# Performance work log

Measured on AMD Instinct MI355X. Metric: run time of the kernel, lower is better.

Reference implementation:

```python
import jax, jax.numpy as jnp
import numpy as np

N = 1000; K = 500; M = N - K          # codeword / info / parity bits
NUE = 4; NBS = 4                      # tx / rx antennas
BPS = 4; RATE = 0.5; NSYM = N // BPS  # 16-QAM, 250 symbols per codeword
NITER = 5                             # BP iterations

# 16-QAM constellation, Gray-coded per axis (Sionna-style), unit energy
_bits = ((np.arange(16)[:, None] >> np.array([3, 2, 1, 0])) & 1).astype(np.float32)
_re = (1 - 2 * _bits[:, 0]) * (2 - (1 - 2 * _bits[:, 2]))
_im = (1 - 2 * _bits[:, 1]) * (2 - (1 - 2 * _bits[:, 3]))
POINTS = jnp.asarray((_re + 1j * _im) / np.sqrt(10.0), dtype=jnp.complex64)  # [16]
LABELS = jnp.asarray(_bits)  # [16,4] bit labels per point


def setup_inputs() -> dict:
    key = jax.random.key(0)
    ks = jax.random.split(key, 5)
    batch = 1000
    # systematic sparse LDPC-like code: H = [P^T | I_M], info-bit degree 3
    rs = np.random.RandomState(0)
    P = np.zeros((K, M), np.int32)
    for i in range(K):
        P[i, rs.choice(M, 3, replace=False)] = 1
    vi, ci = np.nonzero(P)
    vn = np.concatenate([vi, K + np.arange(M)]).astype(np.int32)  # [2000]
    cn = np.concatenate([ci, np.arange(M)]).astype(np.int32)      # [2000]
    b = jax.random.randint(ks[0], (batch, NUE, K), 0, 2, dtype=jnp.int32)
    h_re = jax.random.normal(ks[1], (batch * NSYM, NBS, NUE), jnp.float32)
    h_im = jax.random.normal(ks[2], (batch * NSYM, NBS, NUE), jnp.float32)
    n_re = jax.random.normal(ks[3], (batch * NSYM, NBS), jnp.float32)
    n_im = jax.random.normal(ks[4], (batch * NSYM, NBS), jnp.float32)
    return {"batch_size": batch, "ebno_db": jnp.full((1,), 5.0, jnp.float32),
            "b": b, "P": jnp.asarray(P), "cn_idx": jnp.asarray(cn),
            "vn_idx": jnp.asarray(vn), "h_re": h_re, "h_im": h_im,
            "noise_re": n_re, "noise_im": n_im}


def _forward(batch_size, ebno_db, b, P, cn_idx, vn_idx, h_re, h_im, noise_re, noise_im):
    no = 1.0 / (10.0 ** (ebno_db[0] / 10.0) * BPS * RATE)  # ebnodb2no
    # --- LDPC encode (systematic): c = [b, b@P mod 2] ---
    bf = b.astype(jnp.float32)
    parity = jnp.mod(jnp.round(bf @ P.astype(jnp.float32)), 2.0)
    c = jnp.concatenate([bf, parity], -1)                    # [B,NUE,N]
    # --- QAM mapper ---
    idx = (c.reshape(batch_size, NUE, NSYM, BPS) @ jnp.array([8., 4., 2., 1.], jnp.float32)).astype(jnp.int32)
    x = POINTS[idx]                                          # [B,NUE,NSYM]
    x_f = jnp.transpose(x, (0, 2, 1)).reshape(-1, NUE)       # [B*NSYM,NUE]
    # --- flat fading channel, h ~ CN(0,1), AWGN ---
    h = ((h_re + 1j * h_im) / np.sqrt(2.0)).astype(jnp.complex64)
    w = ((noise_re + 1j * noise_im) * jnp.sqrt(no / 2.0)).astype(jnp.complex64)
    y = jnp.einsum('bij,bj->bi', h, x_f) + w                 # [B*NSYM,NBS]
    # --- LMMSE equalizer: G = H^H (H H^H + no I)^-1, unbiased scaling ---
    A = jnp.einsum('bik,bjk->bij', h, jnp.conj(h)) \
        + no.astype(jnp.complex64) * jnp.eye(NBS, dtype=jnp.complex64)
    Ainv_y = jnp.linalg.solve(A, y[..., None])[..., 0]
    x_raw = jnp.einsum('bij,bi->bj', jnp.conj(h), Ainv_y)    # G y, [B*NSYM,NUE]
    GH = jnp.einsum('bij,bik->bjk', jnp.conj(h), jnp.linalg.solve(A, h))
    d = jnp.real(jnp.diagonal(GH, axis1=1, axis2=2))         # diag(GH), [B*NSYM,NUE]
    x_hat = x_raw / d.astype(jnp.complex64)
    no_eff = jnp.maximum(1.0 / d - 1.0, 1e-12)
    x_hat = jnp.transpose(x_hat.reshape(batch_size, NSYM, NUE), (0, 2, 1))  # [B,NUE,NSYM]
    nvar = jnp.transpose(no_eff.reshape(batch_size, NSYM, NUE), (0, 2, 1))
    # --- max-log demapper, L = log p(b=0)/p(b=1) ---
    metric = -(jnp.abs(x_hat[..., None] - POINTS) ** 2) / nvar[..., None]   # [B,NUE,NSYM,16]
    NEG = jnp.float32(-1e30)
    m5 = metric[..., None, :]                               # [B,NUE,NSYM,1,16]
    lab = LABELS.T[None, None, None]                        # [1,1,1,4,16]
    m0 = jnp.max(jnp.where(lab == 0, m5, NEG), -1)
    m1 = jnp.max(jnp.where(lab == 1, m5, NEG), -1)
    llr = (m0 - m1).reshape(batch_size, NUE, N)
    # --- LDPC BP decoder (sum-product over fixed sparse Tanner graph) ---
    Lch = llr.reshape(batch_size * NUE, N).T                # [N, Bc]
    c2v = jnp.zeros((cn_idx.shape[0], Lch.shape[1]), jnp.float32)  # [E, Bc]
    for _ in range(NITER):
        vtot = Lch.at[vn_idx].add(c2v)                      # Lch + segment_sum(c2v)
        m_vc = vtot[vn_idx] - c2v                           # extrinsic VN->CN
        t = jnp.tanh(jnp.clip(m_vc * 0.5, -9.9, 9.9))
        t = jnp.where(t >= 0, jnp.maximum(t, 1e-7), jnp.minimum(t, -1e-7))
        prod = jax.ops.segment_prod(t, cn_idx, num_segments=M)
        c2v = 2.0 * jnp.arctanh(jnp.clip(prod[cn_idx] / t, -0.999999, 0.999999))
    vtot = Lch.at[vn_idx].add(c2v)
    b_hat = (vtot[:K].T < 0).astype(jnp.float32).reshape(batch_size, NUE, K)
    return bf, b_hat


def reference(batch_size, ebno_db, b, P, cn_idx, vn_idx, h_re, h_im, noise_re, noise_im):
    return _forward(batch_size, ebno_db, b, P, cn_idx, vn_idx,
                    h_re, h_im, noise_re, noise_im)
```

## Files before the change

kernel.cpp:

```cpp
#include <hip/hip_runtime.h>
#include <math.h>

#define KK     500
#define MM     500
#define NNODES 1000
#define NSYM   250
#define NITERS 5
#define MAXVDEG 4
#define EMAX   2048
#define TB     256

__global__ void __launch_bounds__(512)
k_setup(const int* __restrict__ cn, const int* __restrict__ vn, int E,
        const float* __restrict__ ebno, const int* __restrict__ P,
        const int* __restrict__ b, int ncw,
        int* __restrict__ cinfo, int* __restrict__ vlist, int* __restrict__ coff,
        double* __restrict__ nobuf, unsigned* __restrict__ Ppack,
        unsigned* __restrict__ bpack, float* __restrict__ out, int packBlocks) {
  __shared__ int sdeg[512];
  __shared__ int ssc[512];
  __shared__ int scur[512];
  __shared__ int svc[NNODES];
  int tid = threadIdx.x;
  int bx = blockIdx.x;

  if (bx == 0) {
    sdeg[tid] = 0;
    for (int n = tid; n < NNODES; n += 512) svc[n] = 0;
    __syncthreads();
    for (int e = tid; e < E; e += 512) atomicAdd(&sdeg[cn[e]], 1);
    __syncthreads();
    int v = sdeg[tid];
    ssc[tid] = v;
    __syncthreads();
    for (int o = 1; o < 512; o <<= 1) {
      int x = (tid >= o) ? ssc[tid - o] : 0;
      __syncthreads();
      ssc[tid] += x;
      __syncthreads();
    }
    int excl = ssc[tid] - v;
    scur[tid] = excl;
    if (tid < MM) {
      coff[tid] = excl;
      if (tid == MM - 1) coff[MM] = ssc[tid];
    }
    __syncthreads();
    for (int e = tid; e < E; e += 512) {
      int c = cn[e], n = vn[e];
      int slot = atomicAdd(&scur[c], 1);
      cinfo[slot] = (c << 16) | n;
      int t = atomicAdd(&svc[n], 1);
      if (t < MAXVDEG) vlist[n * MAXVDEG + t] = slot;
    }
    if (tid == 0) {
      double no = 1.0 / (pow(10.0, (double)ebno[0] * 0.1) * 2.0);
      nobuf[0] = no;
      nobuf[1] = sqrt(no * 0.5);
    }
    return;
  }

  if (bx <= packBlocks) {
    int id = (bx - 1) * 512 + tid;
    if (id < MM * 16) {
      int j = id >> 4, w = id & 15;
      unsigned word = 0u;
      int base = w * 32;
      for (int bit = 0; bit < 32; ++bit) {
        int i = base + bit;
        if (i < KK && P[i * MM + j] != 0) word |= (1u << bit);
      }
      Ppack[j * 16 + w] = word;
    } else {
      int id2 = id - MM * 16;
      if (id2 < ncw * 16) {
        int cw = id2 >> 4, w = id2 & 15;
        unsigned word = 0u;
        int base = w * 32;
        for (int bit = 0; bit < 32; ++bit) {
          int i = base + bit;
          if (i < KK && b[cw * KK + i] != 0) word |= (1u << bit);
        }
        bpack[cw * 16 + w] = word;
      }
    }
    return;
  }

  int id = (bx - 1 - packBlocks) * 512 + tid;
  if (id < ncw * KK) out[id] = (float)b[id];
}

__device__ __forceinline__ void qam_point(int p, double& re, double& im) {
  const double s = 0.31622776601683794;
  int b0 = (p >> 3) & 1, b1 = (p >> 2) & 1, b2 = (p >> 1) & 1, b3 = p & 1;
  re = (double)((1 - 2 * b0) * (2 - (1 - 2 * b2))) * s;
  im = (double)((1 - 2 * b1) * (2 - (1 - 2 * b3))) * s;
}

__global__ void __launch_bounds__(256, 1)
k_lmmse(const float* __restrict__ h_re, const float* __restrict__ h_im,
        const float* __restrict__ n_re, const float* __restrict__ n_im,
        const double* __restrict__ nobuf,
        const unsigned* __restrict__ bpack, const unsigned* __restrict__ Ppack,
        float* __restrict__ Lch2, int T, int ncw) {
  int t = blockIdx.x * blockDim.x + threadIdx.x;
  if (t >= T) return;
  int bt = t / NSYM, s = t - bt * NSYM;

  double no = nobuf[0];
  double sq = nobuf[1];
  const double is2 = 0.7071067811865475244;

  double Hr[4][4], Hi[4][4];
  {
    const float4* hr4 = (const float4*)h_re;
    const float4* hi4 = (const float4*)h_im;
    #pragma unroll
    for (int i = 0; i < 4; ++i) {
      float4 a = hr4[t * 4 + i], c = hi4[t * 4 + i];
      Hr[i][0] = (double)a.x * is2; Hr[i][1] = (double)a.y * is2;
      Hr[i][2] = (double)a.z * is2; Hr[i][3] = (double)a.w * is2;
      Hi[i][0] = (double)c.x * is2; Hi[i][1] = (double)c.y * is2;
      Hi[i][2] = (double)c.z * is2; Hi[i][3] = (double)c.w * is2;
    }
  }

  double xr[4], xi[4];
  #pragma unroll
  for (int ue = 0; ue < 4; ++ue) {
    const unsigned* bp = bpack + (bt * 4 + ue) * 16;
    int v = 0;
    #pragma unroll
    for (int k = 0; k < 4; ++k) {
      int n = 4 * s + k;
      int bit;
      if (n < KK) {
        bit = (bp[n >> 5] >> (n & 31)) & 1;
      } else {
        const unsigned* pp = Ppack + (n - KK) * 16;
        int cnt = 0;
        #pragma unroll
        for (int w = 0; w < 16; ++w) cnt += __popc(bp[w] & pp[w]);
        bit = cnt & 1;
      }
      v = (v << 1) | bit;
    }
    qam_point(v, xr[ue], xi[ue]);
  }

  double yr[4], yi[4];
  {
    float4 wr = ((const float4*)n_re)[t];
    float4 wi = ((const float4*)n_im)[t];
    float wrv[4] = {wr.x, wr.y, wr.z, wr.w};
    float wiv[4] = {wi.x, wi.y, wi.z, wi.w};
    #pragma unroll
    for (int i = 0; i < 4; ++i) {
      double ar = (double)wrv[i] * sq;
      double ai = (double)wiv[i] * sq;
      #pragma unroll
      for (int j = 0; j < 4; ++j) {
        ar += Hr[i][j] * xr[j] - Hi[i][j] * xi[j];
        ai += Hr[i][j] * xi[j] + Hi[i][j] * xr[j];
      }
      yr[i] = ar; yi[i] = ai;
    }
  }

  auto dotc = [&](int i, int j, double& ar, double& ai) {
    double r = 0.0, m = 0.0;
    #pragma unroll
    for (int k = 0; k < 4; ++k) {
      r += Hr[i][k] * Hr[j][k] + Hi[i][k] * Hi[j][k];
      m += Hi[i][k] * Hr[j][k] - Hr[i][k] * Hi[j][k];
    }
    ar = r; ai = m;
  };
  double a00, a11, a22, a33, dum;
  double a10r, a10i, a20r, a20i, a21r, a21i, a30r, a30i, a31r, a31i, a32r, a32i;
  dotc(0, 0, a00, dum);  a00 += no;
  dotc(1, 0, a10r, a10i);
  dotc(1, 1, a11, dum);  a11 += no;
  dotc(2, 0, a20r, a20i);
  dotc(2, 1, a21r, a21i);
  dotc(2, 2, a22, dum);  a22 += no;
  dotc(3, 0, a30r, a30i);
  dotc(3, 1, a31r, a31i);
  dotc(3, 2, a32r, a32i);
  dotc(3, 3, a33, dum);  a33 += no;

  double L00 = sqrt(a00);
  double i00 = 1.0 / L00;
  double L10r = a10r * i00, L10i = a10i * i00;
  double L20r = a20r * i00, L20i = a20i * i00;
  double L30r = a30r * i00, L30i = a30i * i00;
  double L11 = sqrt(a11 - (L10r * L10r + L10i * L10i));
  double i11 = 1.0 / L11;
  double L21r = (a21r - (L20r * L10r + L20i * L10i)) * i11;
  double L21i = (a21i - (L20i * L10r - L20r * L10i)) * i11;
  double L31r = (a31r - (L30r * L10r + L30i * L10i)) * i11;
  double L31i = (a31i - (L30i * L10r - L30r * L10i)) * i11;
  double L22 = sqrt(a22 - (L20r * L20r + L20i * L20i) - (L21r * L21r + L21i * L21i));
  double i22 = 1.0 / L22;
  double L32r = (a32r - (L30r * L20r + L30i * L20i) - (L31r * L21r + L31i * L21i)) * i22;
  double L32i = (a32i - (L30i * L20r - L30r * L20i) - (L31i * L21r - L31r * L21i)) * i22;
  double L33 = sqrt(a33 - (L30r * L30r + L30i * L30i) - (L31r * L31r + L31i * L31i)
                        - (L32r * L32r + L32i * L32i));
  double i33 = 1.0 / L33;

  #pragma unroll
  for (int j = 0; j < 4; ++j) {
    double u0r = Hr[0][j] * i00,               u0i = Hi[0][j] * i00;
    double u1r = (Hr[1][j] - (L10r * u0r - L10i * u0i)) * i11;
    double u1i = (Hi[1][j] - (L10r * u0i + L10i * u0r)) * i11;
    double u2r = (Hr[2][j] - (L20r * u0r - L20i * u0i) - (L21r * u1r - L21i * u1i)) * i22;
    double u2i = (Hi[2][j] - (L20r * u0i + L20i * u0r) - (L21r * u1i + L21i * u1r)) * i22;
    double u3r = (Hr[3][j] - (L30r * u0r - L30i * u0i) - (L31r * u1r - L31i * u1i)
                           - (L32r * u2r - L32i * u2i)) * i33;
    double u3i = (Hi[3][j] - (L30r * u0i + L30i * u0r) - (L31r * u1i + L31i * u1r)
                           - (L32r * u2i + L32i * u2r)) * i33;
    Hr[0][j] = u0r; Hi[0][j] = u0i; Hr[1][j] = u1r; Hi[1][j] = u1i;
    Hr[2][j] = u2r; Hi[2][j] = u2i; Hr[3][j] = u3r; Hi[3][j] = u3i;
  }
  {
    double v0r = yr[0] * i00,               v0i = yi[0] * i00;
    double v1r = (yr[1] - (L10r * v0r - L10i * v0i)) * i11;
    double v1i = (yi[1] - (L10r * v0i + L10i * v0r)) * i11;
    double v2r = (yr[2] - (L20r * v0r - L20i * v0i) - (L21r * v1r - L21i * v1i)) * i22;
    double v2i = (yi[2] - (L20r * v0i + L20i * v0r) - (L21r * v1i + L21i * v1r)) * i22;
    double v3r = (yr[3] - (L30r * v0r - L30i * v0i) - (L31r * v1r - L31i * v1i)
                        - (L32r * v2r - L32i * v2i)) * i33;
    double v3i = (yi[3] - (L30r * v0i + L30i * v0r) - (L31r * v1i + L31i * v1r)
                        - (L32r * v2i + L32i * v2r)) * i33;
    yr[0] = v0r; yi[0] = v0i; yr[1] = v1r; yi[1] = v1i;
    yr[2] = v2r; yi[2] = v2i; yr[3] = v3r; yi[3] = v3i;
  }

  const float PRT[16] = { 0.31622776601683794f, 0.31622776601683794f, 0.9486832980505138f, 0.9486832980505138f,
                          0.31622776601683794f, 0.31622776601683794f, 0.9486832980505138f, 0.9486832980505138f,
                         -0.31622776601683794f,-0.31622776601683794f,-0.9486832980505138f,-0.9486832980505138f,
                         -0.31622776601683794f,-0.31622776601683794f,-0.9486832980505138f,-0.9486832980505138f };
  const float PIT[16] = { 0.31622776601683794f, 0.9486832980505138f, 0.31622776601683794f, 0.9486832980505138f,
                         -0.31622776601683794f,-0.9486832980505138f,-0.31622776601683794f,-0.9486832980505138f,
                          0.31622776601683794f, 0.9486832980505138f, 0.31622776601683794f, 0.9486832980505138f,
                         -0.31622776601683794f,-0.9486832980505138f,-0.31622776601683794f,-0.9486832980505138f };

  float llr[4][4];
  #pragma unroll
  for (int j = 0; j < 4; ++j) {
    double dj = 0.0, rr = 0.0, ri = 0.0;
    #pragma unroll
    for (int i = 0; i < 4; ++i) {
      dj += Hr[i][j] * Hr[i][j] + Hi[i][j] * Hi[i][j];
      rr += Hr[i][j] * yr[i] + Hi[i][j] * yi[i];
      ri += Hr[i][j] * yi[i] - Hi[i][j] * yr[i];
    }
    float xhr = (float)(rr / dj), xhi = (float)(ri / dj);
    float inoe = (float)(1.0 / fmax(1.0 / dj - 1.0, 1e-12));

    float m0[4] = {-1e30f, -1e30f, -1e30f, -1e30f};
    float m1[4] = {-1e30f, -1e30f, -1e30f, -1e30f};
    #pragma unroll
    for (int p = 0; p < 16; ++p) {
      float dr = xhr - PRT[p], di = xhi - PIT[p];
      float met = -(dr * dr + di * di) * inoe;
      #pragma unroll
      for (int k = 0; k < 4; ++k) {
        if ((p >> (3 - k)) & 1) m1[k] = fmaxf(m1[k], met);
        else                    m0[k] = fmaxf(m0[k], met);
      }
    }
    #pragma unroll
    for (int k = 0; k < 4; ++k) llr[k][j] = m0[k] - m1[k];
  }

  float4* dst = (float4*)(Lch2 + (size_t)bt * (NNODES * 4)) + 4 * s;
  #pragma unroll
  for (int k = 0; k < 4; ++k)
    dst[k] = make_float4(llr[k][0], llr[k][1], llr[k][2], llr[k][3]);
}

__device__ __forceinline__ float tanh_half(float m) {
  float mc = fminf(fmaxf(m, -19.8f), 19.8f);
  float e = __expf(mc);
  float t = 1.0f - __fdividef(2.0f, e + 1.0f);
  return (t >= 0.0f) ? fmaxf(t, 1e-7f) : fminf(t, -1e-7f);
}
__device__ __forceinline__ float ratioW(float P, float t) {
  float r = __fdividef(P, t);
  r = fminf(fmaxf(r, -0.999999f), 0.999999f);
  return __fdividef(1.0f + r, 1.0f - r);
}
__device__ __forceinline__ float t_from_w(float w) {
  w = fminf(fmaxf(w, 2.5109992e-9f), 3.9824784e8f);
  float t = __fdividef(w - 1.0f, w + 1.0f);
  return (t >= 0.0f) ? fmaxf(t, 1e-7f) : fminf(t, -1e-7f);
}
__device__ __forceinline__ float atanh2c(float P, float t) {
  float r = __fdividef(P, t);
  r = fminf(fmaxf(r, -0.999999f), 0.999999f);
  return __logf(__fdividef(1.0f + r, 1.0f - r));
}
__device__ __forceinline__ float4 tanh_half4(float4 m) {
  return make_float4(tanh_half(m.x), tanh_half(m.y), tanh_half(m.z), tanh_half(m.w));
}
__device__ __forceinline__ float4 ratioW4(float4 P, float4 t) {
  return make_float4(ratioW(P.x, t.x), ratioW(P.y, t.y), ratioW(P.z, t.z), ratioW(P.w, t.w));
}
__device__ __forceinline__ float4 tw4(float4 E, float4 A, float4 B) {
  return make_float4(t_from_w(E.x * A.x * B.x), t_from_w(E.y * A.y * B.y),
                     t_from_w(E.z * A.z * B.z), t_from_w(E.w * A.w * B.w));
}

__global__ void __launch_bounds__(256) k_bp(const float* __restrict__ Lch2,
                                            const int* __restrict__ vlist,
                                            const int* __restrict__ coff,
                                            const int* __restrict__ cinfo,
                                            float* __restrict__ out, int E, int ncw) {
  __shared__ float4 sL[NNODES];
  __shared__ float4 sT[EMAX];
  __shared__ float4 sP[512];

  int tid = threadIdx.x;
  int bt = blockIdx.x;

  const float4* src = (const float4*)(Lch2 + (size_t)bt * (NNODES * 4));
  float4 En[2];
  #pragma unroll
  for (int i = 0; i < 4; ++i) {
    int n = tid + TB * i;
    if (n < NNODES) {
      float4 L = src[n];
      sL[n] = L;
      if (i < 2 && n < KK)
        En[i] = make_float4(__expf(fminf(fmaxf(L.x, -55.f), 55.f)),
                            __expf(fminf(fmaxf(L.y, -55.f), 55.f)),
                            __expf(fminf(fmaxf(L.z, -55.f), 55.f)),
                            __expf(fminf(fmaxf(L.w, -55.f), 55.f)));
    }
  }

  #pragma unroll
  for (int i = 0; i < 2; ++i) {
    int n = KK + tid + TB * i;
    if (n < NNODES) {
      int slot = vlist[n * MAXVDEG];
      sT[slot] = tanh_half4(src[n]);
    }
  }

  int pk0[2], pk1[2], pk2[2]; bool iok[2];
  #pragma unroll
  for (int i = 0; i < 2; ++i) {
    int n = tid + TB * i;
    iok[i] = n < KK;
    pk0[i] = pk1[i] = pk2[i] = 0;
    if (iok[i]) {
      int s0 = vlist[n * MAXVDEG], s1 = vlist[n * MAXVDEG + 1], s2 = vlist[n * MAXVDEG + 2];
      pk0[i] = (cinfo[s0] & 0xffff0000) | s0;
      pk1[i] = (cinfo[s1] & 0xffff0000) | s1;
      pk2[i] = (cinfo[s2] & 0xffff0000) | s2;
    }
  }
  int beg0 = coff[tid], end0 = coff[tid + 1];
  bool c1ok = (tid + TB) < MM;
  int beg1 = c1ok ? coff[tid + TB] : 0;
  int end1 = c1ok ? coff[tid + TB + 1] : 0;
  __syncthreads();

  for (int it = 0; it < NITERS; ++it) {
    if (it == 0) {
      #pragma unroll
      for (int i = 0; i < 2; ++i) {
        if (iok[i]) {
          int n = tid + TB * i;
          float4 t = tanh_half4(sL[n]);
          sT[pk0[i] & 0xffff] = t;
          sT[pk1[i] & 0xffff] = t;
          sT[pk2[i] & 0xffff] = t;
        }
      }
    } else {
      #pragma unroll
      for (int i = 0; i < 2; ++i) {
        if (iok[i]) {
          int s0 = pk0[i] & 0xffff, c0 = ((unsigned)pk0[i]) >> 16;
          int s1 = pk1[i] & 0xffff, c1 = ((unsigned)pk1[i]) >> 16;
          int s2 = pk2[i] & 0xffff, c2 = ((unsigned)pk2[i]) >> 16;
          float4 W0 = ratioW4(sP[c0], sT[s0]);
          float4 W1 = ratioW4(sP[c1], sT[s1]);
          float4 W2 = ratioW4(sP[c2], sT[s2]);
          float4 Ev = En[i];
          sT[s0] = tw4(Ev, W1, W2);
          sT[s1] = tw4(Ev, W0, W2);
          sT[s2] = tw4(Ev, W0, W1);
        }
      }
    }
    __syncthreads();
    {
      float px = 1.0f, py = 1.0f, pz = 1.0f, pw = 1.0f;
      for (int e = beg0; e < end0; ++e) {
        float4 tt = sT[e];
        px *= tt.x; py *= tt.y; pz *= tt.z; pw *= tt.w;
      }
      sP[tid] = make_float4(px, py, pz, pw);
      if (c1ok) {
        float qx = 1.0f, qy = 1.0f, qz = 1.0f, qw = 1.0f;
        for (int e = beg1; e < end1; ++e) {
          float4 tt = sT[e];
          qx *= tt.x; qy *= tt.y; qz *= tt.z; qw *= tt.w;
        }
        sP[tid + TB] = make_float4(qx, qy, qz, qw);
      }
    }
    __syncthreads();
  }

  float* o0 = out + (size_t)ncw * KK + (size_t)(bt * 4) * KK;
  float* o1 = o0 + KK;
  float* o2 = o1 + KK;
  float* o3 = o2 + KK;
  #pragma unroll
  for (int i = 0; i < 2; ++i) {
    if (iok[i]) {
      int n = tid + TB * i;
      int s0 = pk0[i] & 0xffff, c0 = ((unsigned)pk0[i]) >> 16;
      int s1 = pk1[i] & 0xffff, c1 = ((unsigned)pk1[i]) >> 16;
      int s2 = pk2[i] & 0xffff, c2 = ((unsigned)pk2[i]) >> 16;
      float4 P0 = sP[c0], P1 = sP[c1], P2 = sP[c2];
      float4 t0 = sT[s0], t1 = sT[s1], t2 = sT[s2];
      float4 L = sL[n];
      float ax = L.x + atanh2c(P0.x, t0.x) + atanh2c(P1.x, t1.x) + atanh2c(P2.x, t2.x);
      float ay = L.y + atanh2c(P0.y, t0.y) + atanh2c(P1.y, t1.y) + atanh2c(P2.y, t2.y);
      float az = L.z + atanh2c(P0.z, t0.z) + atanh2c(P1.z, t1.z) + atanh2c(P2.z, t2.z);
      float aw = L.w + atanh2c(P0.w, t0.w) + atanh2c(P1.w, t1.w) + atanh2c(P2.w, t2.w);
      o0[n] = (ax < 0.0f) ? 1.0f : 0.0f;
      o1[n] = (ay < 0.0f) ? 1.0f : 0.0f;
      o2[n] = (az < 0.0f) ? 1.0f : 0.0f;
      o3[n] = (aw < 0.0f) ? 1.0f : 0.0f;
    }
  }
}

extern "C" void kernel_launch(void* const* d_in, const int* in_sizes, int n_in,
                              void* d_out, int out_size, void* d_ws, size_t ws_size,
                              hipStream_t stream) {
  const float* ebno = (const float*)d_in[1];
  const int*   b    = (const int*)d_in[2];
  const int*   P    = (const int*)d_in[3];
  const int*   cn   = (const int*)d_in[4];
  const int*   vn   = (const int*)d_in[5];
  const float* h_re = (const float*)d_in[6];
  const float* h_im = (const float*)d_in[7];
  const float* nre  = (const float*)d_in[8];
  const float* nim  = (const float*)d_in[9];
  float* out = (float*)d_out;

  int E     = in_sizes[4];
  int batch = in_sizes[2] / (4 * KK);
  int ncw   = batch * 4;
  int T     = batch * NSYM;

  char* ws = (char*)d_ws;
  size_t off = 0;
  auto alloc = [&](size_t bytes) -> void* {
    void* p = ws + off;
    off += (bytes + 255) & ~(size_t)255;
    return p;
  };
  float*    Lch2   = (float*)alloc((size_t)NNODES * ncw * 4);
  unsigned* Ppack  = (unsigned*)alloc((size_t)MM * 16 * 4);
  unsigned* bpack  = (unsigned*)alloc((size_t)ncw * 16 * 4);
  int*      coff   = (int*)alloc((size_t)(MM + 1) * 4);
  int*      cinfo  = (int*)alloc((size_t)EMAX * 4);
  int*      vlist  = (int*)alloc((size_t)NNODES * MAXVDEG * 4);
  double*   nobuf  = (double*)alloc(2 * 8);
  (void)ws_size; (void)n_in; (void)out_size;

  int packItems  = MM * 16 + ncw * 16;
  int packBlocks = (packItems + 511) / 512;
  int bfBlocks   = (ncw * KK + 511) / 512;
  int setupGrid  = 1 + packBlocks + bfBlocks;

  k_setup<<<dim3(setupGrid), dim3(512), 0, stream>>>(cn, vn, E, ebno, P, b, ncw,
                                                     cinfo, vlist, coff, nobuf,
                                                     Ppack, bpack, out, packBlocks);
  k_lmmse<<<dim3((T + TB - 1) / TB), dim3(TB), 0, stream>>>(h_re, h_im, nre, nim, nobuf,
                                                            bpack, Ppack, Lch2, T, ncw);
  k_bp<<<dim3(ncw / 4), dim3(TB), 0, stream>>>(Lch2, vlist, coff, cinfo, out, E, ncw);
}
```

Before: 208.4 us.

## Split BP decoder blocks to two codewords each with float2 layout

The LLR buffer is re-laid out as two float2 planes per group of four codewords, so each BP block decodes two codewords instead of four and twice as many blocks are launched. Shared memory per block shrinks (sL is removed and sT/sP become float2), and channel LLRs are kept in registers. The VN update is algebraically restructured to compute tanh from ratio products with one division per edge instead of separate ratio and tanh conversions. The aim is higher occupancy and more parallelism in the latency-bound BP kernel, at the cost of having the per-block graph setup done twice as often.

```diff
diff --git a/kernel.cpp b/kernel.cpp
--- a/kernel.cpp
+++ b/kernel.cpp
@@ -104,7 +104,7 @@
         const float* __restrict__ n_re, const float* __restrict__ n_im,
         const double* __restrict__ nobuf,
         const unsigned* __restrict__ bpack, const unsigned* __restrict__ Ppack,
-        float* __restrict__ Lch2, int T, int ncw) {
+        float* __restrict__ Lch3, int T, int ncw) {
   int t = blockIdx.x * blockDim.x + threadIdx.x;
   if (t >= T) return;
   int bt = t / NSYM, s = t - bt * NSYM;
@@ -276,10 +276,14 @@
     for (int k = 0; k < 4; ++k) llr[k][j] = m0[k] - m1[k];
   }
 
-  float4* dst = (float4*)(Lch2 + (size_t)bt * (NNODES * 4)) + 4 * s;
-  #pragma unroll
-  for (int k = 0; k < 4; ++k)
-    dst[k] = make_float4(llr[k][0], llr[k][1], llr[k][2], llr[k][3]);
+  float2* pl0 = (float2*)(Lch3 + (size_t)bt * (NNODES * 4));
+  float2* pl1 = pl0 + NNODES;
+  #pragma unroll
+  for (int k = 0; k < 4; ++k) {
+    int node = 4 * s + k;
+    pl0[node] = make_float2(llr[k][0], llr[k][1]);
+    pl1[node] = make_float2(llr[k][2], llr[k][3]);
+  }
 }
 
 __device__ __forceinline__ float tanh_half(float m) {
@@ -288,14 +292,11 @@
   float t = 1.0f - __fdividef(2.0f, e + 1.0f);
   return (t >= 0.0f) ? fmaxf(t, 1e-7f) : fminf(t, -1e-7f);
 }
-__device__ __forceinline__ float ratioW(float P, float t) {
+__device__ __forceinline__ float rclip(float P, float t) {
   float r = __fdividef(P, t);
-  r = fminf(fmaxf(r, -0.999999f), 0.999999f);
-  return __fdividef(1.0f + r, 1.0f - r);
-}
-__device__ __forceinline__ float t_from_w(float w) {
-  w = fminf(fmaxf(w, 2.5109992e-9f), 3.9824784e8f);
-  float t = __fdividef(w - 1.0f, w + 1.0f);
+  return fminf(fmaxf(r, -0.999999f), 0.999999f);
+}
+__device__ __forceinline__ float tfloor(float t) {
   return (t >= 0.0f) ? fmaxf(t, 1e-7f) : fminf(t, -1e-7f);
 }
 __device__ __forceinline__ float atanh2c(float P, float t) {
@@ -303,80 +304,60 @@
   r = fminf(fmaxf(r, -0.999999f), 0.999999f);
   return __logf(__fdividef(1.0f + r, 1.0f - r));
 }
-__device__ __forceinline__ float4 tanh_half4(float4 m) {
-  return make_float4(tanh_half(m.x), tanh_half(m.y), tanh_half(m.z), tanh_half(m.w));
-}
-__device__ __forceinline__ float4 ratioW4(float4 P, float4 t) {
-  return make_float4(ratioW(P.x, t.x), ratioW(P.y, t.y), ratioW(P.z, t.z), ratioW(P.w, t.w));
-}
-__device__ __forceinline__ float4 tw4(float4 E, float4 A, float4 B) {
-  return make_float4(t_from_w(E.x * A.x * B.x), t_from_w(E.y * A.y * B.y),
-                     t_from_w(E.z * A.z * B.z), t_from_w(E.w * A.w * B.w));
-}
-
-__global__ void __launch_bounds__(256) k_bp(const float* __restrict__ Lch2,
+
+__global__ void __launch_bounds__(256) k_bp(const float* __restrict__ Lch3,
                                             const int* __restrict__ vlist,
                                             const int* __restrict__ coff,
                                             const int* __restrict__ cinfo,
                                             float* __restrict__ out, int E, int ncw) {
-  __shared__ float4 sL[NNODES];
-  __shared__ float4 sT[EMAX];
-  __shared__ float4 sP[512];
+  __shared__ float2 sT[EMAX];
+  __shared__ float2 sP[512];
 
   int tid = threadIdx.x;
-  int bt = blockIdx.x;
-
-  const float4* src = (const float4*)(Lch2 + (size_t)bt * (NNODES * 4));
-  float4 En[2];
-  #pragma unroll
-  for (int i = 0; i < 4; ++i) {
+  int pairId = blockIdx.x;
+
+  const float2* src = (const float2*)(Lch3 + (size_t)pairId * (NNODES * 2));
+
+  float2 Ln[2], En[2];
+  int pk0[2], pk1[2], pk2[2]; bool iok[2];
+  #pragma unroll
+  for (int i = 0; i < 2; ++i) {
     int n = tid + TB * i;
-    if (n < NNODES) {
-      float4 L = src[n];
-      sL[n] = L;
-      if (i < 2 && n < KK)
-        En[i] = make_float4(__expf(fminf(fmaxf(L.x, -55.f), 55.f)),
-                            __expf(fminf(fmaxf(L.y, -55.f), 55.f)),
-                            __expf(fminf(fmaxf(L.z, -55.f), 55.f)),
-                            __expf(fminf(fmaxf(L.w, -55.f), 55.f)));
-    }
-  }
-
+    iok[i] = n < KK;
+    Ln[i] = make_float2(0.f, 0.f);
+    En[i] = make_float2(1.f, 1.f);
+    pk0[i] = pk1[i] = pk2[i] = 0;
+    if (iok[i]) {
+      float2 L = src[n];
+      Ln[i] = L;
+      En[i] = make_float2(__expf(fminf(fmaxf(L.x, -55.f), 55.f)),
+                          __expf(fminf(fmaxf(L.y, -55.f), 55.f)));
+      int s0 = vlist[n * MAXVDEG], s1 = vlist[n * MAXVDEG + 1], s2 = vlist[n * MAXVDEG + 2];
+      pk0[i] = (cinfo[s0] & 0xffff0000) | s0;
+      pk1[i] = (cinfo[s1] & 0xffff0000) | s1;
+      pk2[i] = (cinfo[s2] & 0xffff0000) | s2;
+    }
+  }
   #pragma unroll
   for (int i = 0; i < 2; ++i) {
     int n = KK + tid + TB * i;
     if (n < NNODES) {
       int slot = vlist[n * MAXVDEG];
-      sT[slot] = tanh_half4(src[n]);
-    }
-  }
-
-  int pk0[2], pk1[2], pk2[2]; bool iok[2];
-  #pragma unroll
-  for (int i = 0; i < 2; ++i) {
-    int n = tid + TB * i;
-    iok[i] = n < KK;
-    pk0[i] = pk1[i] = pk2[i] = 0;
-    if (iok[i]) {
-      int s0 = vlist[n * MAXVDEG], s1 = vlist[n * MAXVDEG + 1], s2 = vlist[n * MAXVDEG + 2];
-      pk0[i] = (cinfo[s0] & 0xffff0000) | s0;
-      pk1[i] = (cinfo[s1] & 0xffff0000) | s1;
-      pk2[i] = (cinfo[s2] & 0xffff0000) | s2;
+      float2 L = src[n];
+      sT[slot] = make_float2(tanh_half(L.x), tanh_half(L.y));
     }
   }
   int beg0 = coff[tid], end0 = coff[tid + 1];
   bool c1ok = (tid + TB) < MM;
   int beg1 = c1ok ? coff[tid + TB] : 0;
   int end1 = c1ok ? coff[tid + TB + 1] : 0;
-  __syncthreads();
 
   for (int it = 0; it < NITERS; ++it) {
     if (it == 0) {
       #pragma unroll
       for (int i = 0; i < 2; ++i) {
         if (iok[i]) {
-          int n = tid + TB * i;
-          float4 t = tanh_half4(sL[n]);
+          float2 t = make_float2(tanh_half(Ln[i].x), tanh_half(Ln[i].y));
           sT[pk0[i] & 0xffff] = t;
           sT[pk1[i] & 0xffff] = t;
           sT[pk2[i] & 0xffff] = t;
@@ -389,40 +370,49 @@
           int s0 = pk0[i] & 0xffff, c0 = ((unsigned)pk0[i]) >> 16;
           int s1 = pk1[i] & 0xffff, c1 = ((unsigned)pk1[i]) >> 16;
           int s2 = pk2[i] & 0xffff, c2 = ((unsigned)pk2[i]) >> 16;
-          float4 W0 = ratioW4(sP[c0], sT[s0]);
-          float4 W1 = ratioW4(sP[c1], sT[s1]);
-          float4 W2 = ratioW4(sP[c2], sT[s2]);
-          float4 Ev = En[i];
-          sT[s0] = tw4(Ev, W1, W2);
-          sT[s1] = tw4(Ev, W0, W2);
-          sT[s2] = tw4(Ev, W0, W1);
+          float2 P0 = sP[c0], P1 = sP[c1], P2 = sP[c2];
+          float2 t0 = sT[s0], t1 = sT[s1], t2 = sT[s2];
+          float r0 = rclip(P0.x, t0.x), r1 = rclip(P1.x, t1.x), r2 = rclip(P2.x, t2.x);
+          float a0 = 1.f + r0, a1 = 1.f + r1, a2 = 1.f + r2;
+          float b0 = 1.f - r0, b1 = 1.f - r1, b2 = 1.f - r2;
+          float Ex = En[i].x;
+          float A0 = Ex * (a1 * a2), A1 = Ex * (a0 * a2), A2 = Ex * (a0 * a1);
+          float B0 = b1 * b2,        B1 = b0 * b2,        B2 = b0 * b1;
+          float n0x = tfloor(__fdividef(A0 - B0, A0 + B0));
+          float n1x = tfloor(__fdividef(A1 - B1, A1 + B1));
+          float n2x = tfloor(__fdividef(A2 - B2, A2 + B2));
+          float q0 = rclip(P0.y, t0.y), q1 = rclip(P1.y, t1.y), q2 = rclip(P2.y, t2.y);
+          float c0a = 1.f + q0, c1a = 1.f + q1, c2a = 1.f + q2;
+          float d0b = 1.f - q0, d1b = 1.f - q1, d2b = 1.f - q2;
+          float Ey = En[i].y;
+          float C0 = Ey * (c1a * c2a), C1 = Ey * (c0a * c2a), C2 = Ey * (c0a * c1a);
+          float D0 = d1b * d2b,        D1 = d0b * d2b,        D2 = d0b * d1b;
+          float n0y = tfloor(__fdividef(C0 - D0, C0 + D0));
+          float n1y = tfloor(__fdividef(C1 - D1, C1 + D1));
+          float n2y = tfloor(__fdividef(C2 - D2, C2 + D2));
+          sT[s0] = make_float2(n0x, n0y);
+          sT[s1] = make_float2(n1x, n1y);
+          sT[s2] = make_float2(n2x, n2y);
         }
       }
     }
     __syncthreads();
     {
-      float px = 1.0f, py = 1.0f, pz = 1.0f, pw = 1.0f;
-      for (int e = beg0; e < end0; ++e) {
-        float4 tt = sT[e];
-        px *= tt.x; py *= tt.y; pz *= tt.z; pw *= tt.w;
-      }
-      sP[tid] = make_float4(px, py, pz, pw);
+      float px = 1.0f, py = 1.0f;
+      for (int e = beg0; e < end0; ++e) { float2 tt = sT[e]; px *= tt.x; py *= tt.y; }
+      sP[tid] = make_float2(px, py);
       if (c1ok) {
-        float qx = 1.0f, qy = 1.0f, qz = 1.0f, qw = 1.0f;
-        for (int e = beg1; e < end1; ++e) {
-          float4 tt = sT[e];
-          qx *= tt.x; qy *= tt.y; qz *= tt.z; qw *= tt.w;
-        }
-        sP[tid + TB] = make_float4(qx, qy, qz, qw);
-      }
-    }
-    __syncthreads();
-  }
-
-  float* o0 = out + (size_t)ncw * KK + (size_t)(bt * 4) * KK;
+        float qx = 1.0f, qy = 1.0f;
+        for (int e = beg1; e < end1; ++e) { float2 tt = sT[e]; qx *= tt.x; qy *= tt.y; }
+        sP[tid + TB] = make_float2(qx, qy);
+      }
+    }
+    __syncthreads();
+  }
+
+  int cw0 = pairId * 2;
+  float* o0 = out + (size_t)ncw * KK + (size_t)cw0 * KK;
   float* o1 = o0 + KK;
-  float* o2 = o1 + KK;
-  float* o3 = o2 + KK;
   #pragma unroll
   for (int i = 0; i < 2; ++i) {
     if (iok[i]) {
@@ -430,17 +420,13 @@
       int s0 = pk0[i] & 0xffff, c0 = ((unsigned)pk0[i]) >> 16;
       int s1 = pk1[i] & 0xffff, c1 = ((unsigned)pk1[i]) >> 16;
       int s2 = pk2[i] & 0xffff, c2 = ((unsigned)pk2[i]) >> 16;
-      float4 P0 = sP[c0], P1 = sP[c1], P2 = sP[c2];
-      float4 t0 = sT[s0], t1 = sT[s1], t2 = sT[s2];
-      float4 L = sL[n];
+      float2 P0 = sP[c0], P1 = sP[c1], P2 = sP[c2];
+      float2 t0 = sT[s0], t1 = sT[s1], t2 = sT[s2];
+      float2 L = Ln[i];
       float ax = L.x + atanh2c(P0.x, t0.x) + atanh2c(P1.x, t1.x) + atanh2c(P2.x, t2.x);
       float ay = L.y + atanh2c(P0.y, t0.y) + atanh2c(P1.y, t1.y) + atanh2c(P2.y, t2.y);
-      float az = L.z + atanh2c(P0.z, t0.z) + atanh2c(P1.z, t1.z) + atanh2c(P2.z, t2.z);
-      float aw = L.w + atanh2c(P0.w, t0.w) + atanh2c(P1.w, t1.w) + atanh2c(P2.w, t2.w);
       o0[n] = (ax < 0.0f) ? 1.0f : 0.0f;
       o1[n] = (ay < 0.0f) ? 1.0f : 0.0f;
-      o2[n] = (az < 0.0f) ? 1.0f : 0.0f;
-      o3[n] = (aw < 0.0f) ? 1.0f : 0.0f;
     }
   }
 }
@@ -471,7 +457,7 @@
     off += (bytes + 255) & ~(size_t)255;
     return p;
   };
-  float*    Lch2   = (float*)alloc((size_t)NNODES * ncw * 4);
+  float*    Lch3   = (float*)alloc((size_t)NNODES * ncw * 4);
   unsigned* Ppack  = (unsigned*)alloc((size_t)MM * 16 * 4);
   unsigned* bpack  = (unsigned*)alloc((size_t)ncw * 16 * 4);
   int*      coff   = (int*)alloc((size_t)(MM + 1) * 4);
@@ -489,6 +475,6 @@
                                                      cinfo, vlist, coff, nobuf,
                                                      Ppack, bpack, out, packBlocks);
   k_lmmse<<<dim3((T + TB - 1) / TB), dim3(TB), 0, stream>>>(h_re, h_im, nre, nim, nobuf,
-                                                            bpack, Ppack, Lch2, T, ncw);
-  k_bp<<<dim3(ncw / 4), dim3(TB), 0, stream>>>(Lch2, vlist, coff, cinfo, out, E, ncw);
-}
+                                                            bpack, Ppack, Lch3, T, ncw);
+  k_bp<<<dim3(ncw / 2), dim3(TB), 0, stream>>>(Lch3, vlist, coff, cinfo, out, E, ncw);
+}
```

Measured after the change: 195.9 us. -6.0%, faster.
